# Kernel optimization log

Measured on AMD Instinct MI355X. Metric: run time of the kernel, lower is better.

Reference implementation:

```python
import jax, jax.numpy as jnp
import numpy as np
from jax import lax

KSIZE = (7, 7, 7)
SIGMA = (2.0, 2.0, 2.0)


def gaussian_1d(ksize, sigma):
    # matches: exp(-(x - ksize//2 - offset)^2 / (2 sigma^2)), offset=0, normalized
    x = jnp.arange(ksize, dtype=jnp.float32)
    g = jnp.exp(-((x - ksize // 2) ** 2) / (2.0 * sigma ** 2))
    return g / g.sum()


def gaussian_kernel_3d(ksize, sigma):
    k0 = gaussian_1d(ksize[0], sigma[0])
    k1 = gaussian_1d(ksize[1], sigma[1])
    k2 = gaussian_1d(ksize[2], sigma[2])
    # kernel[i,j,l] = k0[i]*k1[j]*k2[l]  (outer product, same as torch code)
    return k0[:, None, None] * k1[None, :, None] * k2[None, None, :]


def setup_inputs() -> dict:
    key = jax.random.key(0)
    x = jax.random.normal(key, (2, 2, 160, 160, 160), dtype=jnp.float32)
    return {"x": x}


def reference(x) -> jnp.ndarray:
    c = x.shape[1]
    k = gaussian_kernel_3d(KSIZE, SIGMA).astype(x.dtype)  # [kD,kH,kW]
    # depthwise weight: [O=C, I/groups=1, kD, kH, kW]
    w = jnp.broadcast_to(k[None, None], (c, 1) + k.shape)
    out = lax.conv_general_dilated(
        x, w,
        window_strides=(1, 1, 1),
        padding="SAME",
        feature_group_count=c,
        dimension_numbers=("NCDHW", "OIDHW", "NCDHW"),
    )
    return out
```

## Files before the change

### kernel.cpp

```cpp
#include <hip/hip_runtime.h>
#include <math.h>

#define DIM 160
#define HT 32
#define ROWS (HT + 6)
#define LROW 168
#define CHUNK 20
#define SLAB4 (DIM * DIM / 4)

struct W7 { float w[7]; };

__global__ __launch_bounds__(512) void blur_wh(const float* __restrict__ in,
                                               float* __restrict__ out, W7 wt) {
    __shared__ float inL[ROWS * LROW];
    __shared__ float tmpL[ROWS * DIM];

    const int tilesH = DIM / HT;
    int b   = blockIdx.x;
    int nc  = b / (DIM * tilesH);
    int rem = b % (DIM * tilesH);
    int d   = rem / tilesH;
    int h0  = (rem % tilesH) * HT;
    int tid = threadIdx.x;

    const float* img = in + ((size_t)nc * DIM + d) * (DIM * DIM);

    for (int i = tid; i < ROWS * 40; i += 512) {
        int r = i / 40, c = i % 40;
        int h = h0 - 3 + r;
        float4 v = make_float4(0.f, 0.f, 0.f, 0.f);
        if (h >= 0 && h < DIM) v = ((const float4*)(img + h * DIM))[c];
        ((float4*)(inL + r * LROW + 4))[c] = v;
    }
    for (int i = tid; i < ROWS * 2; i += 512) {
        int r = i / 2, side = i % 2;
        ((float4*)(inL + r * LROW + (side ? 164 : 0)))[0] =
            make_float4(0.f, 0.f, 0.f, 0.f);
    }
    __syncthreads();

    for (int i = tid; i < ROWS * DIM; i += 512) {
        int r = i / DIM, w = i % DIM;
        const float* p = inL + r * LROW + w + 1;
        float acc = 0.f;
#pragma unroll
        for (int j = 0; j < 7; ++j) acc += wt.w[j] * p[j];
        tmpL[r * DIM + w] = acc;
    }
    __syncthreads();

    float* orow = out + ((size_t)nc * DIM + d) * (DIM * DIM) + (size_t)h0 * DIM;
    for (int i = tid; i < HT * 40; i += 512) {
        int hh = i / 40, c = i % 40;
        float4 acc = make_float4(0.f, 0.f, 0.f, 0.f);
#pragma unroll
        for (int j = 0; j < 7; ++j) {
            float4 t = ((const float4*)(tmpL + (hh + j) * DIM))[c];
            float wj = wt.w[j];
            acc.x += wj * t.x; acc.y += wj * t.y;
            acc.z += wj * t.z; acc.w += wj * t.w;
        }
        ((float4*)(orow + hh * DIM))[c] = acc;
    }
}

__global__ __launch_bounds__(256) void blur_dm(const float4* __restrict__ in,
                                               float4* __restrict__ out, W7 wt) {
    const int sblocks = SLAB4 / 256;
    const int nchunks = DIM / CHUNK;
    int b     = blockIdx.x;
    int sblk  = b % sblocks;
    int chunk = (b / sblocks) % nchunks;
    int ch    = b / (sblocks * nchunks);
    int s4    = sblk * 256 + threadIdx.x;
    int d0    = chunk * CHUNK;
    const size_t base = (size_t)ch * DIM * SLAB4;

    const float4 z4 = make_float4(0.f, 0.f, 0.f, 0.f);
    float4 win[7];
#pragma unroll
    for (int j = 0; j < 6; ++j) {
        int dd = d0 - 3 + j;
        win[j] = (dd >= 0 && dd < DIM) ? in[base + (size_t)dd * SLAB4 + s4] : z4;
    }
#pragma unroll
    for (int k = 0; k < CHUNK; ++k) {
        int dd = d0 + k + 3;
        win[(k + 6) % 7] = (dd < DIM) ? in[base + (size_t)dd * SLAB4 + s4] : z4;
        float4 acc = make_float4(0.f, 0.f, 0.f, 0.f);
#pragma unroll
        for (int j = 0; j < 7; ++j) {
            float wj = wt.w[j];
            float4 v = win[(k + j) % 7];
            acc.x += wj * v.x; acc.y += wj * v.y;
            acc.z += wj * v.z; acc.w += wj * v.w;
        }
        out[base + (size_t)(d0 + k) * SLAB4 + s4] = acc;
    }
}

__global__ void blur3d_naive(const float* __restrict__ in, float* __restrict__ out,
                             W7 wt, int total) {
    int idx = blockIdx.x * blockDim.x + threadIdx.x;
    if (idx >= total) return;
    int w = idx % DIM;
    int h = (idx / DIM) % DIM;
    int d = (idx / (DIM * DIM)) % DIM;
    const float* base = in + (idx - w - h * DIM - d * DIM * DIM);
    float acc = 0.f;
    for (int a = 0; a < 7; ++a) {
        int dd = d + a - 3;
        if (dd < 0 || dd >= DIM) continue;
        for (int bme = 0; bme < 7; ++bme) {
            int hh = h + bme - 3;
            if (hh < 0 || hh >= DIM) continue;
            float wab = wt.w[a] * wt.w[bme];
            for (int c = 0; c < 7; ++c) {
                int ww = w + c - 3;
                if (ww < 0 || ww >= DIM) continue;
                acc += wab * wt.w[c] * base[(dd * DIM + hh) * DIM + ww];
            }
        }
    }
    out[idx] = acc;
}

extern "C" void kernel_launch(void* const* d_in, const int* in_sizes, int n_in,
                              void* d_out, int out_size, void* d_ws, size_t ws_size,
                              hipStream_t stream) {
    const float* x = (const float*)d_in[0];
    float* out = (float*)d_out;
    const int total = out_size;

    W7 wt;
    double s = 0.0;
    for (int i = 0; i < 7; ++i) {
        double v = exp(-((i - 3) * (i - 3)) / 8.0);
        wt.w[i] = (float)v;
        s += v;
    }
    for (int i = 0; i < 7; ++i) wt.w[i] = (float)(wt.w[i] / s);

    if (ws_size >= (size_t)total * sizeof(float)) {
        float* tmp = (float*)d_ws;
        const int nc = total / (DIM * DIM * DIM);
        const int blocksWH = nc * DIM * (DIM / HT);
        blur_wh<<<blocksWH, 512, 0, stream>>>(x, tmp, wt);
        const int blocksD = nc * (DIM / CHUNK) * (SLAB4 / 256);
        blur_dm<<<blocksD, 256, 0, stream>>>(
            (const float4*)tmp, (float4*)out, wt);
    } else {
        blur3d_naive<<<(total + 255) / 256, 256, 0, stream>>>(x, out, wt, total);
    }
}
```

Measured before the change: 53.41 us.

## Replace shared-memory W/H blur with register-marching kernel reading neighbor float4s

The W+H pass no longer stages tiles in LDS. Each thread owns one float4 column and marches down 16 rows. It computes the W blur from three overlapping global float4 loads and keeps a 7-entry register ring for the H blur. This removes the LDS traffic and the two __syncthreads barriers. In exchange, neighbor loads from global memory are redundant (served mostly by cache) and the halo re-read overhead per 16-row chunk is larger than with the old 32-row tiles.

```diff
diff --git a/kernel.cpp b/kernel.cpp
--- a/kernel.cpp
+++ b/kernel.cpp
@@ -2,71 +2,75 @@
 #include <math.h>
 
 #define DIM 160
-#define HT 32
-#define ROWS (HT + 6)
-#define LROW 168
+#define SL4 (DIM * DIM / 4)
+#define CH 16
+#define DPB 8
 #define CHUNK 20
-#define SLAB4 (DIM * DIM / 4)
+#define WHTHREADS (DPB * 40)
 
 struct W7 { float w[7]; };
 
-__global__ __launch_bounds__(512) void blur_wh(const float* __restrict__ in,
-                                               float* __restrict__ out, W7 wt) {
-    __shared__ float inL[ROWS * LROW];
-    __shared__ float tmpL[ROWS * DIM];
+__device__ __forceinline__ void fma4(float4& a, float w, const float4& v) {
+    a.x += w * v.x; a.y += w * v.y; a.z += w * v.z; a.w += w * v.w;
+}
 
-    const int tilesH = DIM / HT;
-    int b   = blockIdx.x;
-    int nc  = b / (DIM * tilesH);
-    int rem = b % (DIM * tilesH);
-    int d   = rem / tilesH;
-    int h0  = (rem % tilesH) * HT;
-    int tid = threadIdx.x;
+__global__ __launch_bounds__(WHTHREADS) void blur_wh_march(
+    const float4* __restrict__ in, float4* __restrict__ out, W7 wt) {
+    const int hchunks = DIM / CH;
+    const int dgroups = DIM / DPB;
+    int b  = blockIdx.x;
+    int hc = b % hchunks;
+    int dg = (b / hchunks) % dgroups;
+    int nc = b / (hchunks * dgroups);
 
-    const float* img = in + ((size_t)nc * DIM + d) * (DIM * DIM);
+    const int c  = threadIdx.x % 40;
+    const int dl = threadIdx.x / 40;
+    const int d  = dg * DPB + dl;
+    const int h0 = hc * CH;
 
-    for (int i = tid; i < ROWS * 40; i += 512) {
-        int r = i / 40, c = i % 40;
-        int h = h0 - 3 + r;
-        float4 v = make_float4(0.f, 0.f, 0.f, 0.f);
-        if (h >= 0 && h < DIM) v = ((const float4*)(img + h * DIM))[c];
-        ((float4*)(inL + r * LROW + 4))[c] = v;
-    }
-    for (int i = tid; i < ROWS * 2; i += 512) {
-        int r = i / 2, side = i % 2;
-        ((float4*)(inL + r * LROW + (side ? 164 : 0)))[0] =
-            make_float4(0.f, 0.f, 0.f, 0.f);
-    }
-    __syncthreads();
+    const float4* sl  = in  + ((size_t)nc * DIM + d) * SL4;
+    float4*       osl = out + ((size_t)nc * DIM + d) * SL4;
 
-    for (int i = tid; i < ROWS * DIM; i += 512) {
-        int r = i / DIM, w = i % DIM;
-        const float* p = inL + r * LROW + w + 1;
-        float acc = 0.f;
+    const float4 z4 = make_float4(0.f, 0.f, 0.f, 0.f);
+    float4 ring[7];
 #pragma unroll
-        for (int j = 0; j < 7; ++j) acc += wt.w[j] * p[j];
-        tmpL[r * DIM + w] = acc;
-    }
-    __syncthreads();
+    for (int j = 0; j < 7; ++j) ring[j] = z4;
 
-    float* orow = out + ((size_t)nc * DIM + d) * (DIM * DIM) + (size_t)h0 * DIM;
-    for (int i = tid; i < HT * 40; i += 512) {
-        int hh = i / 40, c = i % 40;
-        float4 acc = make_float4(0.f, 0.f, 0.f, 0.f);
+    const bool cl = (c >= 1), cr = (c <= 38);
+    const float w0 = wt.w[0], w1 = wt.w[1], w2 = wt.w[2], w3 = wt.w[3],
+                w4 = wt.w[4], w5 = wt.w[5], w6 = wt.w[6];
+
 #pragma unroll
-        for (int j = 0; j < 7; ++j) {
-            float4 t = ((const float4*)(tmpL + (hh + j) * DIM))[c];
-            float wj = wt.w[j];
-            acc.x += wj * t.x; acc.y += wj * t.y;
-            acc.z += wj * t.z; acc.w += wj * t.w;
+    for (int k = 0; k < CH + 6; ++k) {
+        const int hh = h0 + k - 3;
+        float4 nw = z4;
+        if ((unsigned)hh < DIM) {
+            const float4* row = sl + hh * 40;
+            float4 l = cl ? row[c - 1] : z4;
+            float4 m = row[c];
+            float4 r = cr ? row[c + 1] : z4;
+            float f1 = l.y, f2 = l.z, f3 = l.w;
+            float f4_ = m.x, f5 = m.y, f6 = m.z, f7 = m.w;
+            float f8 = r.x, f9 = r.y, f10 = r.z;
+            nw.x = w0*f1 + w1*f2 + w2*f3 + w3*f4_ + w4*f5 + w5*f6 + w6*f7;
+            nw.y = w0*f2 + w1*f3 + w2*f4_ + w3*f5 + w4*f6 + w5*f7 + w6*f8;
+            nw.z = w0*f3 + w1*f4_ + w2*f5 + w3*f6 + w4*f7 + w5*f8 + w6*f9;
+            nw.w = w0*f4_ + w1*f5 + w2*f6 + w3*f7 + w4*f8 + w5*f9 + w6*f10;
         }
-        ((float4*)(orow + hh * DIM))[c] = acc;
+        ring[k % 7] = nw;
+        if (k >= 6) {
+            float4 o = z4;
+#pragma unroll
+            for (int j = 0; j < 7; ++j)
+                fma4(o, wt.w[j], ring[(k + 1 + j) % 7]);
+            osl[(h0 + k - 6) * 40 + c] = o;
+        }
     }
 }
 
 __global__ __launch_bounds__(256) void blur_dm(const float4* __restrict__ in,
                                                float4* __restrict__ out, W7 wt) {
-    const int sblocks = SLAB4 / 256;
+    const int sblocks = SL4 / 256;
     const int nchunks = DIM / CHUNK;
     int b     = blockIdx.x;
     int sblk  = b % sblocks;
@@ -74,28 +78,24 @@
     int ch    = b / (sblocks * nchunks);
     int s4    = sblk * 256 + threadIdx.x;
     int d0    = chunk * CHUNK;
-    const size_t base = (size_t)ch * DIM * SLAB4;
+    const size_t base = (size_t)ch * DIM * SL4;
 
     const float4 z4 = make_float4(0.f, 0.f, 0.f, 0.f);
     float4 win[7];
 #pragma unroll
     for (int j = 0; j < 6; ++j) {
         int dd = d0 - 3 + j;
-        win[j] = (dd >= 0 && dd < DIM) ? in[base + (size_t)dd * SLAB4 + s4] : z4;
+        win[j] = (dd >= 0 && dd < DIM) ? in[base + (size_t)dd * SL4 + s4] : z4;
     }
 #pragma unroll
     for (int k = 0; k < CHUNK; ++k) {
         int dd = d0 + k + 3;
-        win[(k + 6) % 7] = (dd < DIM) ? in[base + (size_t)dd * SLAB4 + s4] : z4;
-        float4 acc = make_float4(0.f, 0.f, 0.f, 0.f);
+        win[(k + 6) % 7] = (dd < DIM) ? in[base + (size_t)dd * SL4 + s4] : z4;
+        float4 acc = z4;
 #pragma unroll
-        for (int j = 0; j < 7; ++j) {
-            float wj = wt.w[j];
-            float4 v = win[(k + j) % 7];
-            acc.x += wj * v.x; acc.y += wj * v.y;
-            acc.z += wj * v.z; acc.w += wj * v.w;
-        }
-        out[base + (size_t)(d0 + k) * SLAB4 + s4] = acc;
+        for (int j = 0; j < 7; ++j)
+            fma4(acc, wt.w[j], win[(k + j) % 7]);
+        out[base + (size_t)(d0 + k) * SL4 + s4] = acc;
     }
 }
 
@@ -111,14 +111,14 @@
     for (int a = 0; a < 7; ++a) {
         int dd = d + a - 3;
         if (dd < 0 || dd >= DIM) continue;
-        for (int bme = 0; bme < 7; ++bme) {
-            int hh = h + bme - 3;
+        for (int bb = 0; bb < 7; ++bb) {
+            int hh = h + bb - 3;
             if (hh < 0 || hh >= DIM) continue;
-            float wab = wt.w[a] * wt.w[bme];
-            for (int c = 0; c < 7; ++c) {
-                int ww = w + c - 3;
+            float wab = wt.w[a] * wt.w[bb];
+            for (int cx = 0; cx < 7; ++cx) {
+                int ww = w + cx - 3;
                 if (ww < 0 || ww >= DIM) continue;
-                acc += wab * wt.w[c] * base[(dd * DIM + hh) * DIM + ww];
+                acc += wab * wt.w[cx] * base[(dd * DIM + hh) * DIM + ww];
             }
         }
     }
@@ -144,10 +144,11 @@
     if (ws_size >= (size_t)total * sizeof(float)) {
         float* tmp = (float*)d_ws;
         const int nc = total / (DIM * DIM * DIM);
-        const int blocksWH = nc * DIM * (DIM / HT);
-        blur_wh<<<blocksWH, 512, 0, stream>>>(x, tmp, wt);
-        const int blocksD = nc * (DIM / CHUNK) * (SLAB4 / 256);
-        blur_dm<<<blocksD, 256, 0, stream>>>(
+        const int gridWH = nc * (DIM / DPB) * (DIM / CH);
+        blur_wh_march<<<gridWH, WHTHREADS, 0, stream>>>(
+            (const float4*)x, (float4*)tmp, wt);
+        const int gridD = nc * (DIM / CHUNK) * (SL4 / 256);
+        blur_dm<<<gridD, 256, 0, stream>>>(
             (const float4*)tmp, (float4*)out, wt);
     } else {
         blur3d_naive<<<(total + 255) / 256, 256, 0, stream>>>(x, out, wt, total);
```

After: 76.21 us. 1.43x slower.
